# Optimization experiments

Hardware: AMD Instinct MI355X
Metric: run time of the kernel (lower is better)

## Reference

```python
import jax, jax.numpy as jnp
import numpy as np

B_IN, C_OUT, K, P, STRIDE, ITERS = 32, 32, 3, 4, 2, 3
PSIZE = P * P
EPS = 1e-08
LAMBDA = 0.001
LN_2PI = float(np.log(2.0 * np.pi))


def _patch(t, K, stride):
    # t: (b, h, w, B, d) -> (b, oh, ow, K, K, B, d)
    b, h, w, B, d = t.shape
    oh = (h - K + 1) // stride
    idxs = jnp.arange(oh)[:, None] * stride + jnp.arange(K)[None, :]  # (oh, K)
    t = t[:, idxs]            # (b, oh, K, w, B, d)
    t = t[:, :, :, idxs]      # (b, oh, K, ow, K, B, d)
    t = jnp.transpose(t, (0, 1, 3, 2, 4, 5, 6))  # (b, oh, ow, K, K, B, d)
    return t, oh, oh


def _em_routing(v, a_in, beta_u, beta_a):
    # v: (b,h,w,Bn,C,psize); a_in: (b,h,w,Bn,1)
    b, h, w, Bn, C, psize = v.shape
    mu = sigma_sq = a_out = None
    for it in range(ITERS):
        if it == 0:
            r = jnp.full((b, h, w, Bn, C), 1.0 / C, dtype=v.dtype) * a_in
        else:
            ln_pjh = -((v - mu) ** 2) / (2.0 * sigma_sq) - 0.5 * jnp.log(sigma_sq) - 0.5 * LN_2PI
            ln_ap = ln_pjh.sum(axis=5) + jnp.log(a_out.reshape(b, h, w, 1, C))
            r = jax.nn.softmax(ln_ap, axis=4)
        r_sum = r.sum(axis=3, keepdims=True)                 # (b,h,w,1,C)
        coeff = (r / (r_sum + EPS))[..., None]               # (b,h,w,Bn,C,1)
        mu = jnp.sum(coeff * v, axis=3, keepdims=True)       # (b,h,w,1,C,psize)
        sigma_sq = jnp.sum(coeff * (v - mu) ** 2, axis=3, keepdims=True)
        r_sum6 = r_sum[..., None]                            # (b,h,w,1,C,1)
        cost_h = (beta_u + 0.5 * jnp.log(sigma_sq)) * r_sum6 # log(sqrt(s)) = 0.5*log(s)
        a_out = jax.nn.sigmoid(LAMBDA * (beta_a - cost_h.sum(axis=5, keepdims=True)))
    return mu.reshape(b, h, w, C, psize), a_out.reshape(b, h, w, C, 1)


def setup_inputs() -> dict:
    key = jax.random.key(0)
    k1, k2, k3 = jax.random.split(key, 3)
    b, h, w = 16, 14, 14
    x = jax.random.normal(k1, (b, h, w, B_IN, PSIZE), dtype=jnp.float32)
    a = jax.random.uniform(k2, (b, h, w, B_IN, 1), dtype=jnp.float32)
    weights = jax.random.normal(k3, (1, 1, 1, K * K * B_IN, C_OUT, P, P), dtype=jnp.float32)
    beta_u = jnp.zeros((C_OUT, 1), dtype=jnp.float32)
    beta_a = jnp.zeros((C_OUT, 1), dtype=jnp.float32)
    return {"x": x, "a": a, "weights": weights, "beta_u": beta_u, "beta_a": beta_a}


def reference(x, a, weights, beta_u, beta_a):
    b = x.shape[0]
    p_in, oh, ow = _patch(x, K, STRIDE)
    a_in, _, _ = _patch(a, K, STRIDE)
    KKB = K * K * B_IN
    p_in = p_in.reshape(b, oh, ow, KKB, PSIZE)
    a_in = a_in.reshape(b, oh, ow, KKB, 1)
    # voting: per-capsule PxP pose matmul with transformation matrices
    pose = p_in.reshape(b, oh, ow, KKB, P, P)
    W = weights.reshape(KKB, C_OUT, P, P)
    v = jnp.einsum('bhwnij,ncjl->bhwncil', pose, W).reshape(b, oh, ow, KKB, C_OUT, PSIZE)
    return _em_routing(v, a_in, beta_u, beta_a)
```

## Files before the change

kernel.cpp:

```cpp
#include <hip/hip_runtime.h>


#define LN2PI 1.8378770664093453f

typedef __attribute__((ext_vector_type(2))) float f32x2;
#define FMA2(a, b, c) __builtin_elementwise_fma((a), (b), (c))
__device__ __forceinline__ f32x2 splat2(float x) { f32x2 r; r.x = x; r.y = x; return r; }

#define DPP_ADD(x, ctrl) \
    ((x) + __int_as_float(__builtin_amdgcn_update_dpp( \
        0, __float_as_int(x), (ctrl), 0xF, 0xF, true)))

__device__ __forceinline__ float sum32(float e) {
    float s = e;
    s = DPP_ADD(s, 0xB1);
    s = DPP_ADD(s, 0x4E);
    s = DPP_ADD(s, 0x141);
    s = DPP_ADD(s, 0x140);
    s += __shfl_xor(s, 16);
    return s;
}

__global__ __launch_bounds__(256)
void wtrans(const float4* __restrict__ W4, float4* __restrict__ Wt)
{
    int idx = blockIdx.x * 256 + threadIdx.x;
    if (idx < 36864) {
        int n = idx >> 7;
        int r = idx & 127;
        int c = r >> 2, q = r & 3;
        Wt[((n * 4 + q) << 5) + c] = W4[idx];
    }
}

__global__ __launch_bounds__(256)
void em_fused(const float* __restrict__ x,
              const float* __restrict__ a,
              const float4* __restrict__ Wt,
              const float* __restrict__ bu,
              const float* __restrict__ ba,
              float* __restrict__ out)
{
    __shared__ __align__(16) float4 pose_s[288 * 4];
    __shared__ float ain_s[288];
    __shared__ float SA[2][32][17];
    __shared__ float SB[2][32][17];
    __shared__ f32x2 php_s[32][9];
    __shared__ f32x2 mh_s[32][9];
    __shared__ float A_s[32];
    __shared__ float AU_s[32];

    const int tid  = threadIdx.x;
    const int wv   = tid >> 6;
    const int lane = tid & 63;
    const int half = (lane >> 5) & 1;
    const int c    = lane & 31;

    const int pos = blockIdx.x;
    const int b   = pos / 36;
    const int rem = pos % 36;
    const int oy  = rem / 6, ox = rem % 6;
    const int iy0 = oy * 2, ix0 = ox * 2;

    {
        const float4* x4 = (const float4*)x;
        for (int idx = tid; idx < 1152; idx += 256) {
            int seg = idx >> 7, u = idx & 127;
            int kh = seg / 3, kw = seg % 3;
            pose_s[idx] = x4[((b * 14 + iy0 + kh) * 14 + (ix0 + kw)) * 128 + u];
        }
        const float4* a4 = (const float4*)a;
        float4* e4 = (float4*)ain_s;
        if (tid < 72) {
            int seg = tid >> 3, u = tid & 7;
            int kh = seg / 3, kw = seg % 3;
            e4[tid] = a4[((b * 14 + iy0 + kh) * 14 + (ix0 + kw)) * 8 + u];
        }
    }
    __syncthreads();

    const int n0 = wv * 72 + half;

    for (int it = 0; it < 3; ++it) {
        f32x2 ph[8], mh[8];
        float Ac = 0.f;
        if (it > 0) {
            #pragma unroll
            for (int j = 0; j < 8; ++j) { ph[j] = php_s[c][j]; mh[j] = mh_s[c][j]; }
            float AU = AU_s[c];
            float m = AU;
            #pragma unroll
            for (int mk = 16; mk >= 1; mk >>= 1)
                m = fmaxf(m, __shfl_xor(m, mk));
            Ac = A_s[c] - m;
        }

        f32x2 s1[8], s2[8];
        #pragma unroll
        for (int j = 0; j < 8; ++j) { s1[j] = splat2(0.f); s2[j] = splat2(0.f); }
        float Racc = 0.f;

        const float4* wp = Wt + (size_t)n0 * 128 + c;
        const float4* pp = pose_s + n0 * 4;
        const float* an  = ain_s + n0;

        #define STEP_BODY(USE_SM)                                              \
        {                                                                      \
            float4 wr0 = wp[0], wr1 = wp[32], wr2 = wp[64], wr3 = wp[96];      \
            float4 pr0 = pp[0], pr1 = pp[1], pr2 = pp[2], pr3 = pp[3];         \
            f32x2 w2[8];                                                       \
            w2[0].x = wr0.x; w2[0].y = wr0.y;  w2[1].x = wr0.z; w2[1].y = wr0.w;\
            w2[2].x = wr1.x; w2[2].y = wr1.y;  w2[3].x = wr1.z; w2[3].y = wr1.w;\
            w2[4].x = wr2.x; w2[4].y = wr2.y;  w2[5].x = wr2.z; w2[5].y = wr2.w;\
            w2[6].x = wr3.x; w2[6].y = wr3.y;  w2[7].x = wr3.z; w2[7].y = wr3.w;\
            f32x2 v2[8];                                                       \
            _Pragma("unroll")                                                  \
            for (int i = 0; i < 4; ++i) {                                      \
                float4 pr = (i == 0) ? pr0 : (i == 1) ? pr1 : (i == 2) ? pr2 : pr3; \
                _Pragma("unroll")                                              \
                for (int lp = 0; lp < 2; ++lp) {                               \
                    f32x2 t = splat2(pr.x) * w2[0 + lp];                       \
                    t = FMA2(splat2(pr.y), w2[2 + lp], t);                     \
                    t = FMA2(splat2(pr.z), w2[4 + lp], t);                     \
                    t = FMA2(splat2(pr.w), w2[6 + lp], t);                     \
                    v2[i * 2 + lp] = t;                                        \
                }                                                              \
            }                                                                  \
            float r;                                                           \
            if (USE_SM) {                                                      \
                f32x2 acc2 = splat2(0.f);                                      \
                acc2.x = Ac;                                                   \
                _Pragma("unroll")                                              \
                for (int j = 0; j < 8; ++j) {                                  \
                    f32x2 t = FMA2(ph[j], v2[j], mh[j]);                       \
                    acc2 = FMA2(t, v2[j], acc2);                               \
                }                                                              \
                float e = __expf(acc2.x + acc2.y);                             \
                float ssum = sum32(e);                                         \
                r = __fdividef(e, ssum + 1e-30f);                              \
            } else {                                                           \
                r = an[2 * s] * 0.03125f;                                      \
            }                                                                  \
            Racc += r;                                                         \
            f32x2 rr = splat2(r);                                              \
            _Pragma("unroll")                                                  \
            for (int j = 0; j < 8; ++j) {                                      \
                f32x2 rv = rr * v2[j];                                         \
                s1[j] = s1[j] + rv;                                            \
                s2[j] = FMA2(rv, v2[j], s2[j]);                                \
            }                                                                  \
            wp += 256;                                                         \
            pp += 8;                                                           \
        }

        if (it == 0) {
            for (int s = 0; s < 36; ++s) STEP_BODY(false)
        } else {
            for (int s = 0; s < 36; ++s) STEP_BODY(true)
        }
        #undef STEP_BODY

        #pragma unroll
        for (int j = 0; j < 8; ++j) {
            s1[j].x += __shfl_xor(s1[j].x, 32);
            s1[j].y += __shfl_xor(s1[j].y, 32);
            s2[j].x += __shfl_xor(s2[j].x, 32);
            s2[j].y += __shfl_xor(s2[j].y, 32);
        }
        Racc += __shfl_xor(Racc, 32);

        if (wv >= 2) {
            const int row = wv - 2;
            if (half == 0) {
                #pragma unroll
                for (int j = 0; j < 8; ++j) {
                    SA[row][c][2 * j]     = s1[j].x;
                    SA[row][c][2 * j + 1] = s1[j].y;
                }
                SA[row][c][16] = Racc;
            } else {
                #pragma unroll
                for (int j = 0; j < 8; ++j) {
                    SB[row][c][2 * j]     = s2[j].x;
                    SB[row][c][2 * j + 1] = s2[j].y;
                }
            }
        }
        __syncthreads();
        if (wv < 2) {
            if (half == 0) {
                #pragma unroll
                for (int j = 0; j < 8; ++j) {
                    SA[wv][c][2 * j]     += s1[j].x;
                    SA[wv][c][2 * j + 1] += s1[j].y;
                }
                SA[wv][c][16] += Racc;
            } else {
                #pragma unroll
                for (int j = 0; j < 8; ++j) {
                    SB[wv][c][2 * j]     += s2[j].x;
                    SB[wv][c][2 * j + 1] += s2[j].y;
                }
            }
        }
        __syncthreads();

        {
            const int cf = tid >> 3, k2 = tid & 7;
            float R = SA[0][cf][16] + SA[1][cf][16];
            float rinv = __fdividef(1.f, R + 1e-8f);
            float muv[2];
            float tpart = 0.f, Ks = 0.f;
            #pragma unroll
            for (int t2 = 0; t2 < 2; ++t2) {
                int k = k2 + t2 * 8;
                float sv1 = SA[0][cf][k] + SA[1][cf][k];
                float sv2 = SB[0][cf][k] + SB[1][cf][k];
                float mu  = sv1 * rinv;
                float sig = fmaf(-mu, mu, sv2 * rinv);
                sig = fmaxf(sig, 1e-30f);
                float p = __fdividef(0.5f, sig);
                muv[t2] = mu;
                if (it < 2) {
                    ((float*)&php_s[cf][0])[k] = -p;
                    ((float*)&mh_s[cf][0])[k]  = 2.f * p * mu;
                }
                tpart += __logf(sig);
                Ks = fmaf(p * mu, mu, Ks);
            }
            #pragma unroll
            for (int mk = 4; mk >= 1; mk >>= 1) {
                tpart += __shfl_xor(tpart, mk);
                Ks    += __shfl_xor(Ks, mk);
            }
            float cost = R * fmaf(0.5f, tpart, 16.f * bu[cf]);
            float aout = __fdividef(1.f, 1.f + __expf(-(0.001f * (ba[cf] - cost))));

            if (it < 2) {
                if (k2 == 0) {
                    float Afold = __logf(aout) - 0.5f * tpart - 8.0f * LN2PI - Ks;
                    A_s[cf]  = Afold;
                    AU_s[cf] = Afold + Ks;
                }
            } else {
                out[(size_t)pos * 512 + cf * 16 + k2]     = muv[0];
                out[(size_t)pos * 512 + cf * 16 + k2 + 8] = muv[1];
                if (k2 == 0)
                    out[294912 + pos * 32 + cf] = aout;
            }
        }
        __syncthreads();
    }
}

#define NB 288
#define LNSTEP 36
__global__ __launch_bounds__(256, 2)
void convcaps_em_legacy(const float* __restrict__ x, const float* __restrict__ a,
                        const float* __restrict__ W, const float* __restrict__ bu,
                        const float* __restrict__ ba, float* __restrict__ out)
{
    __shared__ __align__(16) float pose_s[NB * 16];
    __shared__ __align__(16) float ain_s[NB];
    __shared__ float S1w[4][32][17];
    __shared__ float S2w[4][32][17];
    __shared__ float Rw[4][32];
    __shared__ float mu_s[32][17];
    __shared__ float p_s[32][17];
    __shared__ float A_s[32];

    const int tid = threadIdx.x, wv = tid >> 6, lane = tid & 63;
    const int half = (lane >> 5) & 1, c = lane & 31;
    const int bid = blockIdx.x, b = bid / 36, rem = bid % 36;
    const int oy = rem / 6, ox = rem % 6, iy0 = oy * 2, ix0 = ox * 2;
    {
        const float4* x4 = (const float4*)x;
        float4* d4 = (float4*)pose_s;
        for (int idx = tid; idx < 1152; idx += 256) {
            int seg = idx >> 7, u = idx & 127, kh = seg / 3, kw = seg % 3;
            d4[idx] = x4[((b * 14 + iy0 + kh) * 14 + (ix0 + kw)) * 128 + u];
        }
        const float4* a4 = (const float4*)a;
        float4* e4 = (float4*)ain_s;
        if (tid < 72) {
            int seg = tid >> 3, u = tid & 7, kh = seg / 3, kw = seg % 3;
            e4[tid] = a4[((b * 14 + iy0 + kh) * 14 + (ix0 + kw)) * 8 + u];
        }
    }
    __syncthreads();
    const float4* W4 = (const float4*)W;
    float muh[16], ph[16], Ac = 0.0f;
    #pragma unroll
    for (int i = 0; i < 16; ++i) { muh[i] = 0.0f; ph[i] = 0.0f; }
    for (int iter = 0; iter < 3; ++iter) {
        if (iter > 0) {
            #pragma unroll
            for (int il = 0; il < 16; ++il) { muh[il] = mu_s[c][il]; ph[il] = p_s[c][il]; }
            Ac = A_s[c];
        }
        float S1[16], S2[16], Racc = 0.0f;
        #pragma unroll
        for (int i = 0; i < 16; ++i) { S1[i] = 0.0f; S2[i] = 0.0f; }
        for (int s = 0; s < LNSTEP; ++s) {
            const int n = wv * 72 + 2 * s + half;
            float wreg[16], preg[16];
            const float4* wp = W4 + (size_t)(n * 32 + c) * 4;
            float4 w0 = wp[0], w1 = wp[1], w2 = wp[2], w3 = wp[3];
            wreg[0]=w0.x; wreg[1]=w0.y; wreg[2]=w0.z; wreg[3]=w0.w;
            wreg[4]=w1.x; wreg[5]=w1.y; wreg[6]=w1.z; wreg[7]=w1.w;
            wreg[8]=w2.x; wreg[9]=w2.y; wreg[10]=w2.z; wreg[11]=w2.w;
            wreg[12]=w3.x; wreg[13]=w3.y; wreg[14]=w3.z; wreg[15]=w3.w;
            const float4* pp = (const float4*)&pose_s[n * 16];
            float4 p0 = pp[0], p1 = pp[1], p2 = pp[2], p3 = pp[3];
            preg[0]=p0.x; preg[1]=p0.y; preg[2]=p0.z; preg[3]=p0.w;
            preg[4]=p1.x; preg[5]=p1.y; preg[6]=p1.z; preg[7]=p1.w;
            preg[8]=p2.x; preg[9]=p2.y; preg[10]=p2.z; preg[11]=p2.w;
            preg[12]=p3.x; preg[13]=p3.y; preg[14]=p3.z; preg[15]=p3.w;
            float v[16];
            #pragma unroll
            for (int i = 0; i < 4; ++i)
                #pragma unroll
                for (int l = 0; l < 4; ++l) {
                    float acc = preg[i*4+0] * wreg[l];
                    acc = fmaf(preg[i*4+1], wreg[4+l], acc);
                    acc = fmaf(preg[i*4+2], wreg[8+l], acc);
                    acc = fmaf(preg[i*4+3], wreg[12+l], acc);
                    v[i*4+l] = acc;
                }
            float r;
            if (iter == 0) r = ain_s[n] * 0.03125f;
            else {
                float acc = 0.0f;
                #pragma unroll
                for (int il = 0; il < 16; ++il) { float d = v[il]-muh[il]; acc = fmaf(-ph[il], d*d, acc); }
                float lnap = Ac + acc, m = lnap;
                #pragma unroll
                for (int mk = 16; mk >= 1; mk >>= 1) m = fmaxf(m, __shfl_xor(m, mk));
                float e = __expf(lnap - m), ssum = e;
                #pragma unroll
                for (int mk = 16; mk >= 1; mk >>= 1) ssum += __shfl_xor(ssum, mk);
                r = __fdividef(e, ssum);
            }
            Racc += r;
            #pragma unroll
            for (int il = 0; il < 16; ++il) { float rv = r * v[il]; S1[il] += rv; S2[il] = fmaf(rv, v[il], S2[il]); }
        }
        #pragma unroll
        for (int il = 0; il < 16; ++il) { S1[il] += __shfl_xor(S1[il], 32); S2[il] += __shfl_xor(S2[il], 32); }
        Racc += __shfl_xor(Racc, 32);
        if (half == 0) {
            #pragma unroll
            for (int il = 0; il < 16; ++il) { S1w[wv][c][il] = S1[il]; S2w[wv][c][il] = S2[il]; }
            Rw[wv][c] = Racc;
        }
        __syncthreads();
        {
            const int c2 = tid >> 3, k = tid & 7;
            float R = Rw[0][c2] + Rw[1][c2] + Rw[2][c2] + Rw[3][c2];
            float rinv = __fdividef(1.0f, R + 1e-8f);
            float muv[2], pv[2], tpart = 0.0f;
            #pragma unroll
            for (int t2 = 0; t2 < 2; ++t2) {
                int il = k + t2 * 8;
                float s1 = S1w[0][c2][il]+S1w[1][c2][il]+S1w[2][c2][il]+S1w[3][c2][il];
                float s2 = S2w[0][c2][il]+S2w[1][c2][il]+S2w[2][c2][il]+S2w[3][c2][il];
                float mu = s1 * rinv;
                float sig = fmaf(-mu, mu, s2 * rinv);
                sig = fmaxf(sig, 1e-30f);
                muv[t2] = mu; pv[t2] = __fdividef(0.5f, sig); tpart += __logf(sig);
            }
            #pragma unroll
            for (int mk = 4; mk >= 1; mk >>= 1) tpart += __shfl_xor(tpart, mk);
            float cost = R * fmaf(0.5f, tpart, 16.0f * bu[c2]);
            float aout = __fdividef(1.0f, 1.0f + __expf(-(0.001f * (ba[c2] - cost))));
            if (iter < 2) {
                #pragma unroll
                for (int t2 = 0; t2 < 2; ++t2) { int il = k + t2*8; mu_s[c2][il] = muv[t2]; p_s[c2][il] = pv[t2]; }
                if (k == 0) A_s[c2] = __logf(aout) - 0.5f * tpart - 8.0f * LN2PI;
            } else {
                #pragma unroll
                for (int t2 = 0; t2 < 2; ++t2) { int il = k + t2*8; out[(size_t)bid*512 + c2*16 + il] = muv[t2]; }
                if (k == 0) out[294912 + bid * 32 + c2] = aout;
            }
        }
        __syncthreads();
    }
}

extern "C" void kernel_launch(void* const* d_in, const int* in_sizes, int n_in,
                              void* d_out, int out_size, void* d_ws, size_t ws_size,
                              hipStream_t stream) {
    (void)in_sizes; (void)n_in; (void)out_size;
    const float* x  = (const float*)d_in[0];
    const float* a  = (const float*)d_in[1];
    const float* w  = (const float*)d_in[2];
    const float* bu = (const float*)d_in[3];
    const float* ba = (const float*)d_in[4];
    float* out = (float*)d_out;
    float* wsf = (float*)d_ws;

    if (ws_size >= (size_t)147456 * 4) {
        float* Wt = wsf;
        hipLaunchKernelGGL(wtrans, dim3(144), dim3(256), 0, stream,
                           (const float4*)w, (float4*)Wt);
        hipLaunchKernelGGL(em_fused, dim3(576), dim3(256), 0, stream,
                           x, a, (const float4*)Wt, bu, ba, out);
    } else {
        hipLaunchKernelGGL(convcaps_em_legacy, dim3(576), dim3(256), 0, stream,
                           x, a, w, bu, ba, out);
    }
}
```

Measured before the change: 85.56 us.

## Double-buffer weight loads in routing loop and fold log2e into exp2

```diff
diff --git a/kernel.cpp b/kernel.cpp
--- a/kernel.cpp
+++ b/kernel.cpp
@@ -2,6 +2,7 @@
 
 
 #define LN2PI 1.8378770664093453f
+#define LOG2E 1.4426950408889634f
 
 typedef __attribute__((ext_vector_type(2))) float f32x2;
 #define FMA2(a, b, c) __builtin_elementwise_fma((a), (b), (c))
@@ -33,7 +34,7 @@
     }
 }
 
-__global__ __launch_bounds__(256)
+__global__ __launch_bounds__(256, 2)
 void em_fused(const float* __restrict__ x,
               const float* __restrict__ a,
               const float4* __restrict__ Wt,
@@ -69,12 +70,10 @@
             int kh = seg / 3, kw = seg % 3;
             pose_s[idx] = x4[((b * 14 + iy0 + kh) * 14 + (ix0 + kw)) * 128 + u];
         }
-        const float4* a4 = (const float4*)a;
-        float4* e4 = (float4*)ain_s;
-        if (tid < 72) {
-            int seg = tid >> 3, u = tid & 7;
+        for (int idx = tid; idx < 288; idx += 256) {
+            int seg = idx >> 5, bi = idx & 31;
             int kh = seg / 3, kw = seg % 3;
-            e4[tid] = a4[((b * 14 + iy0 + kh) * 14 + (ix0 + kw)) * 8 + u];
+            ain_s[idx] = a[((b * 14 + iy0 + kh) * 14 + (ix0 + kw)) * 32 + bi] * 0.03125f;
         }
     }
     __syncthreads();
@@ -104,15 +103,15 @@
         const float4* pp = pose_s + n0 * 4;
         const float* an  = ain_s + n0;
 
-        #define STEP_BODY(USE_SM)                                              \
+        #define COMP(W0, W1, W2, W3, AIN_EXPR, USE_SM)                         \
         {                                                                      \
-            float4 wr0 = wp[0], wr1 = wp[32], wr2 = wp[64], wr3 = wp[96];      \
             float4 pr0 = pp[0], pr1 = pp[1], pr2 = pp[2], pr3 = pp[3];         \
+            pp += 8;                                                           \
             f32x2 w2[8];                                                       \
-            w2[0].x = wr0.x; w2[0].y = wr0.y;  w2[1].x = wr0.z; w2[1].y = wr0.w;\
-            w2[2].x = wr1.x; w2[2].y = wr1.y;  w2[3].x = wr1.z; w2[3].y = wr1.w;\
-            w2[4].x = wr2.x; w2[4].y = wr2.y;  w2[5].x = wr2.z; w2[5].y = wr2.w;\
-            w2[6].x = wr3.x; w2[6].y = wr3.y;  w2[7].x = wr3.z; w2[7].y = wr3.w;\
+            w2[0].x = W0.x; w2[0].y = W0.y;  w2[1].x = W0.z; w2[1].y = W0.w;   \
+            w2[2].x = W1.x; w2[2].y = W1.y;  w2[3].x = W1.z; w2[3].y = W1.w;   \
+            w2[4].x = W2.x; w2[4].y = W2.y;  w2[5].x = W2.z; w2[5].y = W2.w;   \
+            w2[6].x = W3.x; w2[6].y = W3.y;  w2[7].x = W3.z; w2[7].y = W3.w;   \
             f32x2 v2[8];                                                       \
             _Pragma("unroll")                                                  \
             for (int i = 0; i < 4; ++i) {                                      \
@@ -135,11 +134,11 @@
                     f32x2 t = FMA2(ph[j], v2[j], mh[j]);                       \
                     acc2 = FMA2(t, v2[j], acc2);                               \
                 }                                                              \
-                float e = __expf(acc2.x + acc2.y);                             \
+                float e = __builtin_amdgcn_exp2f(acc2.x + acc2.y);             \
                 float ssum = sum32(e);                                         \
                 r = __fdividef(e, ssum + 1e-30f);                              \
             } else {                                                           \
-                r = an[2 * s] * 0.03125f;                                      \
+                r = (AIN_EXPR);                                                \
             }                                                                  \
             Racc += r;                                                         \
             f32x2 rr = splat2(r);                                              \
@@ -149,16 +148,31 @@
                 s1[j] = s1[j] + rv;                                            \
                 s2[j] = FMA2(rv, v2[j], s2[j]);                                \
             }                                                                  \
-            wp += 256;                                                         \
-            pp += 8;                                                           \
-        }
-
+        }
+
+        float4 A0 = wp[0], A1 = wp[32], A2 = wp[64], A3 = wp[96];
         if (it == 0) {
-            for (int s = 0; s < 36; ++s) STEP_BODY(false)
+            for (int s = 0; s < 36; s += 2) {
+                const float4* w1p = wp + 256;
+                float4 B0 = w1p[0], B1 = w1p[32], B2 = w1p[64], B3 = w1p[96];
+                COMP(A0, A1, A2, A3, an[2 * s], false);
+                const float4* w2p = wp + 512;
+                A0 = w2p[0]; A1 = w2p[32]; A2 = w2p[64]; A3 = w2p[96];
+                COMP(B0, B1, B2, B3, an[2 * s + 2], false);
+                wp += 512;
+            }
         } else {
-            for (int s = 0; s < 36; ++s) STEP_BODY(true)
-        }
-        #undef STEP_BODY
+            for (int s = 0; s < 36; s += 2) {
+                const float4* w1p = wp + 256;
+                float4 B0 = w1p[0], B1 = w1p[32], B2 = w1p[64], B3 = w1p[96];
+                COMP(A0, A1, A2, A3, 0.f, true);
+                const float4* w2p = wp + 512;
+                A0 = w2p[0]; A1 = w2p[32]; A2 = w2p[64]; A3 = w2p[96];
+                COMP(B0, B1, B2, B3, 0.f, true);
+                wp += 512;
+            }
+        }
+        #undef COMP
 
         #pragma unroll
         for (int j = 0; j < 8; ++j) {
@@ -222,8 +236,8 @@
                 float p = __fdividef(0.5f, sig);
                 muv[t2] = mu;
                 if (it < 2) {
-                    ((float*)&php_s[cf][0])[k] = -p;
-                    ((float*)&mh_s[cf][0])[k]  = 2.f * p * mu;
+                    ((float*)&php_s[cf][0])[k] = -p * LOG2E;
+                    ((float*)&mh_s[cf][0])[k]  = 2.f * p * mu * LOG2E;
                 }
                 tpart += __logf(sig);
                 Ks = fmaf(p * mu, mu, Ks);
@@ -239,8 +253,8 @@
             if (it < 2) {
                 if (k2 == 0) {
                     float Afold = __logf(aout) - 0.5f * tpart - 8.0f * LN2PI - Ks;
-                    A_s[cf]  = Afold;
-                    AU_s[cf] = Afold + Ks;
+                    A_s[cf]  = Afold * LOG2E;
+                    AU_s[cf] = (Afold + Ks) * LOG2E;
                 }
             } else {
                 out[(size_t)pos * 512 + cf * 16 + k2]     = muv[0];
@@ -399,7 +413,7 @@
     float* out = (float*)d_out;
     float* wsf = (float*)d_ws;
 
-    if (ws_size >= (size_t)147456 * 4) {
+    if (ws_size >= (size_t)(147456 + 8192) * 4) {
         float* Wt = wsf;
         hipLaunchKernelGGL(wtrans, dim3(144), dim3(256), 0, stream,
                            (const float4*)w, (float4*)Wt);
```

New measurement: 89.30 us. 1.04x slower.
